# Kernel optimization log

Measured on AMD Instinct MI355X. Metric: run time of the kernel, lower is better.

The kernel has to match this reference:

```python
import jax, jax.numpy as jnp
import numpy as np

NUM_HEADS = 16

def setup_inputs() -> dict:
    key = jax.random.key(0)
    ks = jax.random.split(key, 5)
    E = 1024
    x = jax.random.normal(ks[0], (2, 2048, E), dtype=jnp.float32)
    w_in = jax.random.normal(ks[1], (3 * E, E), dtype=jnp.float32) * (E ** -0.5)
    b_in = jax.random.normal(ks[2], (3 * E,), dtype=jnp.float32) * 0.02
    w_out = jax.random.normal(ks[3], (E, E), dtype=jnp.float32) * (E ** -0.5)
    b_out = jax.random.normal(ks[4], (E,), dtype=jnp.float32) * 0.02
    return {"x": x, "w_in": w_in, "b_in": b_in, "w_out": w_out, "b_out": b_out}


def reference(x, w_in, b_in, w_out, b_out):
    B, N, E = x.shape
    H = NUM_HEADS
    Dh = E // H
    # fused QKV projection (torch Linear: x @ W^T + b)
    qkv = x @ w_in.T + b_in                      # [B, N, 3E]
    q, k, v = jnp.split(qkv, 3, axis=-1)
    # [B, H, N, Dh]
    q = q.reshape(B, N, H, Dh).transpose(0, 2, 1, 3)
    k = k.reshape(B, N, H, Dh).transpose(0, 2, 1, 3)
    v = v.reshape(B, N, H, Dh).transpose(0, 2, 1, 3)
    scale = Dh ** -0.5
    scores = jnp.einsum("bhqd,bhkd->bhqk", q, k) * scale  # [B, H, N, N]
    attn = jax.nn.softmax(scores, axis=-1)
    out = jnp.einsum("bhqk,bhkd->bhqd", attn, v)          # [B, H, N, Dh]
    out = out.transpose(0, 2, 1, 3).reshape(B, N, E)
    return out @ w_out.T + b_out
```

## Files before the change

kernel.cpp:

```cpp
#include <hip/hip_runtime.h>


typedef __bf16 bf16;
typedef __bf16 bf16x8 __attribute__((ext_vector_type(8)));
typedef __bf16 bf16x4 __attribute__((ext_vector_type(4)));
typedef float  f32x4  __attribute__((ext_vector_type(4)));

#define MFMA16(a, b, c) __builtin_amdgcn_mfma_f32_16x16x32_bf16((a), (b), (c), 0, 0, 0)

#define SC2 0.18033688011112042f

__device__ __forceinline__ void gld_lds16(const void* g, void* l) {
  __builtin_amdgcn_global_load_lds((const __attribute__((address_space(1))) void*)g,
                                   (__attribute__((address_space(3))) void*)l,
                                   16, 0, 0);
}

__global__ __launch_bounds__(256) void cast3_kernel(
    const float* __restrict__ x, const float* __restrict__ wi,
    const float* __restrict__ wo, bf16* __restrict__ xb,
    bf16* __restrict__ wib, bf16* __restrict__ wob) {
  const int i = (blockIdx.x * 256 + threadIdx.x) * 4;
  const float* s; bf16* d; int off;
  if (i < 4194304)      { s = x;  d = xb;  off = i; }
  else if (i < 7340032) { s = wi; d = wib; off = i - 4194304; }
  else                  { s = wo; d = wob; off = i - 7340032; }
  const float4 v = *(const float4*)(s + off);
  bf16x4 o;
  o[0] = (bf16)v.x; o[1] = (bf16)v.y; o[2] = (bf16)v.z; o[3] = (bf16)v.w;
  *(bf16x4*)(d + off) = o;
}

__global__ __launch_bounds__(256) void gemm_qkv_kernel(
    const bf16* __restrict__ A,
    const bf16* __restrict__ B,
    const float* __restrict__ bias,
    bf16* __restrict__ qb, bf16* __restrict__ kb, bf16* __restrict__ vb) {
  constexpr int K = 1024;
  __shared__ __align__(16) char smem[128 * 136 * 2];
  bf16* As = (bf16*)smem;
  bf16* Bs = (bf16*)(smem + 8192);
  const int tid  = threadIdx.x;
  const int lane = tid & 63;
  const int wave = tid >> 6;
  const int m0 = blockIdx.y * 128;
  const int n0 = blockIdx.x * 128;
  const int r_ = tid >> 2;
  const int k_ = (tid & 3) * 8;
  const int lr = lane & 15, lg = lane >> 4;
  const int wm = (wave >> 1) * 64, wn = (wave & 1) * 64;

  f32x4 acc[4][4];
#pragma unroll
  for (int i = 0; i < 4; ++i)
#pragma unroll
    for (int j = 0; j < 4; ++j) acc[i][j] = (f32x4){0.f, 0.f, 0.f, 0.f};

  for (int k0 = 0; k0 < K; k0 += 32) {
    __syncthreads();
    gld_lds16(A + (size_t)(m0 + r_) * K + k0 + k_,      (char*)As + tid * 16);
    gld_lds16(A + (size_t)(m0 + 64 + r_) * K + k0 + k_, (char*)As + 4096 + tid * 16);
    gld_lds16(B + (size_t)(n0 + r_) * K + k0 + k_,      (char*)Bs + tid * 16);
    gld_lds16(B + (size_t)(n0 + 64 + r_) * K + k0 + k_, (char*)Bs + 4096 + tid * 16);
    __syncthreads();

    bf16x8 af[4], bfr[4];
#pragma unroll
    for (int i = 0; i < 4; ++i)
      af[i] = *(const bf16x8*)((const char*)As + (size_t)((wm + i * 16 + lr) * 32 + lg * 8) * 2);
#pragma unroll
    for (int j = 0; j < 4; ++j)
      bfr[j] = *(const bf16x8*)((const char*)Bs + (size_t)((wn + j * 16 + lr) * 32 + lg * 8) * 2);
#pragma unroll
    for (int i = 0; i < 4; ++i)
#pragma unroll
      for (int j = 0; j < 4; ++j) acc[i][j] = MFMA16(af[i], bfr[j], acc[i][j]);
  }

  if (n0 < 2048) {
    const int isq = (n0 < 1024);
#pragma unroll
    for (int j = 0; j < 4; ++j) {
      const int col = n0 + wn + j * 16 + lr;
      const float bv = bias[col];
      const int wi = col & 1023;
      const int h = wi >> 6, d = wi & 63;
      bf16* dst = isq ? qb : kb;
      const float scl = isq ? SC2 : 1.0f;
#pragma unroll
      for (int i = 0; i < 4; ++i) {
#pragma unroll
        for (int r = 0; r < 4; ++r) {
          const int row = m0 + wm + i * 16 + lg * 4 + r;
          const int bb = row >> 11, nn = row & 2047;
          dst[((size_t)(bb * 16 + h) * 2048 + nn) * 64 + d] =
              (bf16)((acc[i][j][r] + bv) * scl);
        }
      }
    }
  } else {
    __syncthreads();
    bf16* Vt = (bf16*)smem;
#pragma unroll
    for (int j = 0; j < 4; ++j) {
      const int c = wn + j * 16 + lr;
      const float bv = bias[n0 + c];
#pragma unroll
      for (int i = 0; i < 4; ++i) {
#pragma unroll
        for (int r = 0; r < 4; ++r) {
          const int rr = wm + i * 16 + lg * 4 + r;
          Vt[c * 136 + rr] = (bf16)(acc[i][j][r] + bv);
        }
      }
    }
    __syncthreads();
    const int wi0 = n0 - 2048;
    const int bb = m0 >> 11, nn0 = m0 & 2047;
#pragma unroll
    for (int pass = 0; pass < 8; ++pass) {
      const int c = pass * 16 + (tid >> 4);
      const int nof = (tid & 15) * 8;
      const int wi = wi0 + c;
      const int h = wi >> 6, d = wi & 63;
      *(bf16x8*)(vb + ((size_t)(bb * 16 + h) * 64 + d) * 2048 + nn0 + nof) =
          *(const bf16x8*)(Vt + c * 136 + nof);
    }
  }
}

__global__ __launch_bounds__(256) void flash_attn_kernel(
    const bf16* __restrict__ q, const bf16* __restrict__ k,
    const bf16* __restrict__ vt, bf16* __restrict__ o) {
  __shared__ bf16 Ks[2][64 * 64];
  __shared__ bf16 Vs[2][64 * 64];
  __shared__ bf16 Pl[4][2][16 * 72];

  const int tid  = threadIdx.x;
  const int lane = tid & 63;
  const int wave = tid >> 6;
  const int lr = lane & 15, lg = lane >> 4;
  const int qt = blockIdx.x;
  const int bh = blockIdx.y;
  const bf16* qp = q  + (size_t)bh * (2048 * 64);
  const bf16* kp = k  + (size_t)bh * (2048 * 64);
  const bf16* vp = vt + (size_t)bh * (64 * 2048);
  const int q0 = qt * 128 + wave * 32;

  int srow[2], scol[2];
#pragma unroll
  for (int p = 0; p < 2; ++p) {
    const int L = p * 4096 + tid * 16;
    srow[p] = L >> 7;
    scol[p] = ((L & 127) ^ ((srow[p] & 7) << 4)) >> 1;
  }

  bf16x8 qf[2][2];
#pragma unroll
  for (int qi = 0; qi < 2; ++qi)
#pragma unroll
    for (int t = 0; t < 2; ++t)
      qf[qi][t] = *(const bf16x8*)(qp + (size_t)(q0 + qi * 16 + lr) * 64 + t * 32 + lg * 8);

  f32x4 oacc[2][4];
#pragma unroll
  for (int qi = 0; qi < 2; ++qi)
#pragma unroll
    for (int j = 0; j < 4; ++j) oacc[qi][j] = (f32x4){0.f, 0.f, 0.f, 0.f};
  float lrow[2][4];
#pragma unroll
  for (int qi = 0; qi < 2; ++qi)
#pragma unroll
    for (int r = 0; r < 4; ++r) lrow[qi][r] = 0.f;

#pragma unroll
  for (int p = 0; p < 2; ++p) {
    const int L = p * 4096 + tid * 16;
    gld_lds16(kp + (size_t)srow[p] * 64 + scol[p],       (char*)Ks[0] + L);
    gld_lds16(vp + (size_t)srow[p] * 2048 + 0 + scol[p], (char*)Vs[0] + L);
  }
  __syncthreads();

  int buf = 0;
  for (int t = 0; t < 32; ++t) {
    if (t + 1 < 32) {
      const int nkv = t * 64 + 64;
#pragma unroll
      for (int p = 0; p < 2; ++p) {
        const int L = p * 4096 + tid * 16;
        gld_lds16(kp + (size_t)(nkv + srow[p]) * 64 + scol[p], (char*)Ks[buf ^ 1] + L);
        gld_lds16(vp + (size_t)srow[p] * 2048 + nkv + scol[p], (char*)Vs[buf ^ 1] + L);
      }
    }

    f32x4 s[2][4];
#pragma unroll
    for (int qi = 0; qi < 2; ++qi)
#pragma unroll
      for (int sub = 0; sub < 4; ++sub) s[qi][sub] = (f32x4){0.f, 0.f, 0.f, 0.f};
    __builtin_amdgcn_s_setprio(1);
#pragma unroll
    for (int sub = 0; sub < 4; ++sub) {
#pragma unroll
      for (int tt = 0; tt < 2; ++tt) {
        const int row = sub * 16 + lr;
        const int byte = (row << 7) + (((tt * 32 + lg * 8) << 1) ^ ((row & 7) << 4));
        bf16x8 kf = *(const bf16x8*)((const char*)Ks[buf] + byte);
#pragma unroll
        for (int qi = 0; qi < 2; ++qi) s[qi][sub] = MFMA16(qf[qi][tt], kf, s[qi][sub]);
      }
    }
    __builtin_amdgcn_s_setprio(0);

#pragma unroll
    for (int qi = 0; qi < 2; ++qi) {
      bf16* pl = &Pl[wave][qi][0];
#pragma unroll
      for (int sub = 0; sub < 4; ++sub) {
#pragma unroll
        for (int r = 0; r < 4; ++r) {
          const float p = exp2f(s[qi][sub][r]);
          lrow[qi][r] += p;
          pl[(lg * 4 + r) * 72 + sub * 16 + lr] = (bf16)p;
        }
      }
    }
    bf16x8 pa[2][2];
#pragma unroll
    for (int qi = 0; qi < 2; ++qi)
#pragma unroll
      for (int kk = 0; kk < 2; ++kk)
        pa[qi][kk] = *(const bf16x8*)(&Pl[wave][qi][0] + lr * 72 + kk * 32 + lg * 8);

    __builtin_amdgcn_s_setprio(1);
#pragma unroll
    for (int j = 0; j < 4; ++j) {
#pragma unroll
      for (int kk = 0; kk < 2; ++kk) {
        const int row = j * 16 + lr;
        const int byte = (row << 7) + (((kk * 32 + lg * 8) << 1) ^ ((row & 7) << 4));
        bf16x8 vf = *(const bf16x8*)((const char*)Vs[buf] + byte);
#pragma unroll
        for (int qi = 0; qi < 2; ++qi) oacc[qi][j] = MFMA16(pa[qi][kk], vf, oacc[qi][j]);
      }
    }
    __builtin_amdgcn_s_setprio(0);

    __syncthreads();
    buf ^= 1;
  }

#pragma unroll
  for (int m_ = 1; m_ <= 8; m_ <<= 1)
#pragma unroll
    for (int qi = 0; qi < 2; ++qi)
#pragma unroll
      for (int r = 0; r < 4; ++r)
        lrow[qi][r] += __shfl_xor(lrow[qi][r], m_, 64);

  const int b = bh >> 4, h = bh & 15;
#pragma unroll
  for (int qi = 0; qi < 2; ++qi) {
    float inv[4];
#pragma unroll
    for (int r = 0; r < 4; ++r) inv[r] = 1.f / lrow[qi][r];
#pragma unroll
    for (int j = 0; j < 4; ++j) {
#pragma unroll
      for (int r = 0; r < 4; ++r) {
        const int qrow = q0 + qi * 16 + lg * 4 + r;
        o[((size_t)(b * 2048 + qrow)) * 1024 + h * 64 + j * 16 + lr] =
            (bf16)(oacc[qi][j][r] * inv[r]);
      }
    }
  }
}

__global__ __launch_bounds__(256) void gemm_out_kernel(
    const bf16* __restrict__ A,
    const bf16* __restrict__ B,
    const float* __restrict__ bias,
    float* __restrict__ out) {
  constexpr int K = 1024;
  __shared__ bf16 As[128 * 32];
  __shared__ bf16 Bs[128 * 32];
  const int tid  = threadIdx.x;
  const int lane = tid & 63;
  const int wave = tid >> 6;
  const int m0 = blockIdx.y * 128;
  const int n0 = blockIdx.x * 128;
  const int r_ = tid >> 2;
  const int k_ = (tid & 3) * 8;
  const int lr = lane & 15, lg = lane >> 4;
  const int wm = (wave >> 1) * 64, wn = (wave & 1) * 64;

  f32x4 acc[4][4];
#pragma unroll
  for (int i = 0; i < 4; ++i)
#pragma unroll
    for (int j = 0; j < 4; ++j) acc[i][j] = (f32x4){0.f, 0.f, 0.f, 0.f};

  for (int k0 = 0; k0 < K; k0 += 32) {
    __syncthreads();
    gld_lds16(A + (size_t)(m0 + r_) * K + k0 + k_,      (char*)As + tid * 16);
    gld_lds16(A + (size_t)(m0 + 64 + r_) * K + k0 + k_, (char*)As + 4096 + tid * 16);
    gld_lds16(B + (size_t)(n0 + r_) * K + k0 + k_,      (char*)Bs + tid * 16);
    gld_lds16(B + (size_t)(n0 + 64 + r_) * K + k0 + k_, (char*)Bs + 4096 + tid * 16);
    __syncthreads();

    bf16x8 af[4], bfr[4];
#pragma unroll
    for (int i = 0; i < 4; ++i)
      af[i] = *(const bf16x8*)((const char*)As + (size_t)((wm + i * 16 + lr) * 32 + lg * 8) * 2);
#pragma unroll
    for (int j = 0; j < 4; ++j)
      bfr[j] = *(const bf16x8*)((const char*)Bs + (size_t)((wn + j * 16 + lr) * 32 + lg * 8) * 2);
#pragma unroll
    for (int i = 0; i < 4; ++i)
#pragma unroll
      for (int j = 0; j < 4; ++j) acc[i][j] = MFMA16(af[i], bfr[j], acc[i][j]);
  }

#pragma unroll
  for (int j = 0; j < 4; ++j) {
    const int col = n0 + wn + j * 16 + lr;
    const float bv = bias[col];
#pragma unroll
    for (int i = 0; i < 4; ++i) {
#pragma unroll
      for (int r = 0; r < 4; ++r) {
        const int row = m0 + wm + i * 16 + lg * 4 + r;
        out[(size_t)row * 1024 + col] = acc[i][j][r] + bv;
      }
    }
  }
}

extern "C" void kernel_launch(void* const* d_in, const int* in_sizes, int n_in,
                              void* d_out, int out_size, void* d_ws, size_t ws_size,
                              hipStream_t stream) {
  const float* x     = (const float*)d_in[0];
  const float* w_in  = (const float*)d_in[1];
  const float* b_in  = (const float*)d_in[2];
  const float* w_out = (const float*)d_in[3];
  const float* b_out = (const float*)d_in[4];
  float* out = (float*)d_out;

  char* ws = (char*)d_ws;
  const size_t MB = 1ull << 20;
  bf16* xb  = (bf16*)(ws + 0 * MB);
  bf16* wib = (bf16*)(ws + 8 * MB);
  bf16* wob = (bf16*)(ws + 14 * MB);
  bf16* qb  = (bf16*)(ws + 16 * MB);
  bf16* kb  = (bf16*)(ws + 24 * MB);
  bf16* vb  = (bf16*)(ws + 32 * MB);
  bf16* ab  = (bf16*)(ws + 40 * MB);

  cast3_kernel<<<dim3(8192), dim3(256), 0, stream>>>(x, w_in, w_out, xb, wib, wob);
  gemm_qkv_kernel<<<dim3(24, 32), dim3(256), 0, stream>>>(xb, wib, b_in, qb, kb, vb);
  flash_attn_kernel<<<dim3(16, 32), dim3(256), 0, stream>>>(qb, kb, vb, ab);
  gemm_out_kernel<<<dim3(8, 32), dim3(256), 0, stream>>>(ab, wob, b_out, out);
}
```

Before: 227.1 us.

## Transpose QK^T MFMA, pack P stores, compute row sums via MFMA with ones

Swaps the MFMA operand order for the score computation so each lane holds four consecutive key columns of one query row. Those four exp values can then be packed into bf16 pairs with v_cvt_pk_bf16_f32 and written to LDS as a single 8-byte store, replacing four scalar 2-byte stores. The softmax denominator is now accumulated by an extra MFMA of P against a vector of ones, which removes the per-element scalar adds and the final cross-lane shuffle reduction. The cost is four extra MFMAs per tile, and the row sum is now taken from the bf16-rounded P rather than the fp32 exponentials.

Measured after the change: 219.6 us. 1.03x faster.

```diff
diff --git a/kernel.cpp b/kernel.cpp
--- a/kernel.cpp
+++ b/kernel.cpp
@@ -162,16 +162,18 @@
     for (int t = 0; t < 2; ++t)
       qf[qi][t] = *(const bf16x8*)(qp + (size_t)(q0 + qi * 16 + lr) * 64 + t * 32 + lg * 8);
 
+  bf16x8 ones;
+#pragma unroll
+  for (int i = 0; i < 8; ++i) ones[i] = (bf16)1.0f;
+
   f32x4 oacc[2][4];
 #pragma unroll
   for (int qi = 0; qi < 2; ++qi)
 #pragma unroll
     for (int j = 0; j < 4; ++j) oacc[qi][j] = (f32x4){0.f, 0.f, 0.f, 0.f};
-  float lrow[2][4];
-#pragma unroll
-  for (int qi = 0; qi < 2; ++qi)
-#pragma unroll
-    for (int r = 0; r < 4; ++r) lrow[qi][r] = 0.f;
+  f32x4 lacc[2];
+#pragma unroll
+  for (int qi = 0; qi < 2; ++qi) lacc[qi] = (f32x4){0.f, 0.f, 0.f, 0.f};
 
 #pragma unroll
   for (int p = 0; p < 2; ++p) {
@@ -207,7 +209,7 @@
         const int byte = (row << 7) + (((tt * 32 + lg * 8) << 1) ^ ((row & 7) << 4));
         bf16x8 kf = *(const bf16x8*)((const char*)Ks[buf] + byte);
 #pragma unroll
-        for (int qi = 0; qi < 2; ++qi) s[qi][sub] = MFMA16(qf[qi][tt], kf, s[qi][sub]);
+        for (int qi = 0; qi < 2; ++qi) s[qi][sub] = MFMA16(kf, qf[qi][tt], s[qi][sub]);
       }
     }
     __builtin_amdgcn_s_setprio(0);
@@ -217,12 +219,15 @@
       bf16* pl = &Pl[wave][qi][0];
 #pragma unroll
       for (int sub = 0; sub < 4; ++sub) {
-#pragma unroll
-        for (int r = 0; r < 4; ++r) {
-          const float p = exp2f(s[qi][sub][r]);
-          lrow[qi][r] += p;
-          pl[(lg * 4 + r) * 72 + sub * 16 + lr] = (bf16)p;
-        }
+        const float e0 = exp2f(s[qi][sub][0]);
+        const float e1 = exp2f(s[qi][sub][1]);
+        const float e2 = exp2f(s[qi][sub][2]);
+        const float e3 = exp2f(s[qi][sub][3]);
+        unsigned p01, p23;
+        asm("v_cvt_pk_bf16_f32 %0, %1, %2" : "=v"(p01) : "v"(e0), "v"(e1));
+        asm("v_cvt_pk_bf16_f32 %0, %1, %2" : "=v"(p23) : "v"(e2), "v"(e3));
+        uint2 w; w.x = p01; w.y = p23;
+        *(uint2*)(pl + lr * 72 + sub * 16 + lg * 4) = w;
       }
     }
     bf16x8 pa[2][2];
@@ -244,26 +249,23 @@
         for (int qi = 0; qi < 2; ++qi) oacc[qi][j] = MFMA16(pa[qi][kk], vf, oacc[qi][j]);
       }
     }
+#pragma unroll
+    for (int qi = 0; qi < 2; ++qi)
+#pragma unroll
+      for (int kk = 0; kk < 2; ++kk)
+        lacc[qi] = MFMA16(pa[qi][kk], ones, lacc[qi]);
     __builtin_amdgcn_s_setprio(0);
 
     __syncthreads();
     buf ^= 1;
   }
-
-#pragma unroll
-  for (int m_ = 1; m_ <= 8; m_ <<= 1)
-#pragma unroll
-    for (int qi = 0; qi < 2; ++qi)
-#pragma unroll
-      for (int r = 0; r < 4; ++r)
-        lrow[qi][r] += __shfl_xor(lrow[qi][r], m_, 64);
 
   const int b = bh >> 4, h = bh & 15;
 #pragma unroll
   for (int qi = 0; qi < 2; ++qi) {
     float inv[4];
 #pragma unroll
-    for (int r = 0; r < 4; ++r) inv[r] = 1.f / lrow[qi][r];
+    for (int r = 0; r < 4; ++r) inv[r] = 1.f / lacc[qi][r];
 #pragma unroll
     for (int j = 0; j < 4; ++j) {
 #pragma unroll
```
